# Kernel tuning notes

Measured on AMD Instinct MI355X. Metric: run time of the kernel, lower is better.

## Reference

```python
import jax, jax.numpy as jnp
import numpy as np

N = 40962  # icosphere level-6 vertex count
EPS = 1e-5

def setup_inputs() -> dict:
    key = jax.random.key(0)
    ks = jax.random.split(key, 8)
    x = jax.random.normal(ks[0], (N, 3), dtype=jnp.float32)
    neigh_orders = jax.random.randint(ks[1], (N * 7,), 0, N, dtype=jnp.int32)
    s0 = 1.0 / np.sqrt(21.0)
    sm = 1.0 / np.sqrt(896.0)
    return {
        "x": x,
        "neigh_orders": neigh_orders,
        "W0": jax.random.uniform(ks[2], (21, 128), jnp.float32, -s0, s0),
        "b0": jax.random.uniform(ks[3], (128,), jnp.float32, -s0, s0),
        "g0": jnp.ones((128,), jnp.float32),
        "be0": jnp.zeros((128,), jnp.float32),
        "Wm": jax.random.uniform(ks[4], (14, 896, 128), jnp.float32, -sm, sm),
        "bm": jax.random.uniform(ks[5], (14, 128), jnp.float32, -sm, sm),
        "gm": jnp.ones((14, 128), jnp.float32),
        "bem": jnp.zeros((14, 128), jnp.float32),
        "Wl": jax.random.uniform(ks[6], (896, 36), jnp.float32, -sm, sm),
        "bl": jax.random.uniform(ks[7], (36,), jnp.float32, -sm, sm),
    }

def _bs(x, idx, W, b):
    # gather 7 fixed ring neighbors per node, flatten, dense linear
    mat = x[idx].reshape(x.shape[0], -1)  # [N, 7*in_feats]
    return mat @ W + b

def _bn_train(h, g, be):
    # BatchNorm1d in training mode: biased variance over the node/batch dim
    mu = jnp.mean(h, axis=0)
    var = jnp.var(h, axis=0)
    return g * (h - mu) * jax.lax.rsqrt(var + EPS) + be

def reference(x, neigh_orders, W0, b0, g0, be0, Wm, bm, gm, bem, Wl, bl):
    idx = neigh_orders
    h = jax.nn.relu(_bn_train(_bs(x, idx, W0, b0), g0, be0))  # [N, 128]

    def step(h, params):
        W, b, g, be = params
        h = jax.nn.relu(_bn_train(_bs(h, idx, W, b), g, be))
        return h, None

    h, _ = jax.lax.scan(step, h, (Wm, bm, gm, bem))  # 14 identical 128->128 blocks
    out = _bs(h, idx, Wl, bl)  # [N, num_classes]
    return out
```

## Files before the change

### kernel.cpp

```cpp
#include <hip/hip_runtime.h>

typedef _Float16 f16x8 __attribute__((ext_vector_type(8)));
typedef float f32x4 __attribute__((ext_vector_type(4)));

#define EPS 1e-5f

__device__ __forceinline__ short f2h(float x) {
    _Float16 h = (_Float16)x;
    union { _Float16 h; short s; } u;
    u.h = h;
    return u.s;
}

__global__ void prep_kernel(const float* __restrict__ Wm, const float* __restrict__ Wl,
                            short* __restrict__ WtM, short* __restrict__ WtF,
                            float* __restrict__ stats) {
    const long T1 = 14L * 896 * 128;
    const long T2 = 48L * 896;
    const long T3 = 15L * 256;
    long i = (long)blockIdx.x * blockDim.x + threadIdx.x;
    if (i < T1) {
        long l = i / (896 * 128);
        long r = i % (896 * 128);
        long k = r >> 7;
        long f = r & 127;
        WtM[l * 114688 + f * 896 + k] = f2h(Wm[i]);
    } else if (i < T1 + T2) {
        long j = i - T1;
        long f = j / 896;
        long k = j % 896;
        WtF[j] = (f < 36) ? f2h(Wl[k * 36 + f]) : (short)0;
    } else if (i < T1 + T2 + T3) {
        stats[i - T1 - T2] = 0.0f;
    }
}

#define L0_NB 16
__global__ __launch_bounds__(256) void layer0_kernel(
        const float* __restrict__ x, const int* __restrict__ idx,
        const float* __restrict__ W0, const float* __restrict__ b0,
        short* __restrict__ hlin, float* __restrict__ stats, int N) {
    __shared__ float sW[21 * 128];
    __shared__ float sX[L0_NB * 21];
    __shared__ float sStat[256];
    const int tid = threadIdx.x;
    for (int i = tid; i < 21 * 128; i += 256) sW[i] = W0[i];
    const int f = tid & 127;
    const int half = tid >> 7;
    const float bf = b0[f];
    float s = 0.f, ss = 0.f;
    const int ntiles = (N + L0_NB - 1) / L0_NB;
    for (int t = blockIdx.x; t < ntiles; t += gridDim.x) {
        const int n0 = t * L0_NB;
        __syncthreads();
        for (int i = tid; i < L0_NB * 21; i += 256) {
            int ni = i / 21;
            int k = i - ni * 21;
            int j = k / 3;
            int c = k - j * 3;
            int n = n0 + ni;
            if (n >= N) n = N - 1;
            sX[i] = x[(long)idx[n * 7 + j] * 3 + c];
        }
        __syncthreads();
#pragma unroll
        for (int ni = 0; ni < 8; ++ni) {
            int node = n0 + half * 8 + ni;
            if (node >= N) break;
            float acc = bf;
#pragma unroll
            for (int k = 0; k < 21; ++k)
                acc = fmaf(sX[(half * 8 + ni) * 21 + k], sW[k * 128 + f], acc);
            hlin[(long)node * 128 + f] = f2h(acc);
            s += acc;
            ss += acc * acc;
        }
    }
    __syncthreads();
    if (half == 1) { sStat[f] = s; sStat[128 + f] = ss; }
    __syncthreads();
    if (half == 0) {
        atomicAdd(&stats[f], s + sStat[f]);
        atomicAdd(&stats[128 + f], ss + sStat[128 + f]);
    }
}

__global__ __launch_bounds__(256, 3) void gemm_mid_kernel(
        const short* __restrict__ hprev, const int* __restrict__ idx,
        const short* __restrict__ Wt, const float* __restrict__ bvec,
        const float* __restrict__ g, const float* __restrict__ be,
        const float* __restrict__ statsIn,
        short* __restrict__ hlin, float* __restrict__ statsOut,
        int N, float invN) {
    __shared__ short sA[64 * 136];
    __shared__ short sB[128 * 136];
    __shared__ float sAux[256];

    const int tid = threadIdx.x;
    const int wave = tid >> 6;
    const int lane = tid & 63;
    const int quad = lane >> 4;
    const int l16 = lane & 15;
    const int wm = wave & 1;
    const int wf = wave >> 1;
    const int m0 = blockIdx.x * 64;
    const int t16 = tid >> 4;
    const int fb = (tid & 15) * 8;

    if (tid < 128) {
        float mu = statsIn[tid] * invN;
        float var = statsIn[128 + tid] * invN - mu * mu;
        float rs = rsqrtf(var + EPS);
        float sc = g[tid] * rs;
        sAux[tid] = sc;
        sAux[128 + tid] = be[tid] - mu * sc;
    }
    __syncthreads();
    float scR[8], shR[8];
#pragma unroll
    for (int e = 0; e < 8; ++e) {
        scR[e] = sAux[fb + e];
        shR[e] = sAux[128 + fb + e];
    }

    f32x4 acc[2][4];
#pragma unroll
    for (int ni = 0; ni < 4; ++ni) {
        float bv0 = bvec[wf * 64 + ni * 16 + l16];
#pragma unroll
        for (int mi = 0; mi < 2; ++mi) {
            acc[mi][ni][0] = bv0; acc[mi][ni][1] = bv0; acc[mi][ni][2] = bv0; acc[mi][ni][3] = bv0;
        }
    }

    f16x8 av[4];
    f16x8 bv[8];

    auto issueA = [&](int j) {
#pragma unroll
        for (int it = 0; it < 4; ++it) {
            int nl = t16 + it * 16;
            int n = m0 + nl;
            n = (n < N) ? n : (N - 1);
            long row = idx[n * 7 + j];
            av[it] = *(const f16x8*)&hprev[row * 128 + fb];
        }
    };
    auto issueB = [&](int j) {
#pragma unroll
        for (int it = 0; it < 8; ++it) {
            int ff = t16 + it * 16;
            bv[it] = *(const f16x8*)&Wt[(long)ff * 896 + j * 128 + fb];
        }
    };
    auto writeA = [&]() {
#pragma unroll
        for (int it = 0; it < 4; ++it) {
            int nl = t16 + it * 16;
            f16x8 hv = av[it];
            union { short sh8[8]; f16x8 v; } u;
#pragma unroll
            for (int e = 0; e < 8; ++e) {
                float v = (float)hv[e];
                u.sh8[e] = f2h(fmaxf(fmaf(v, scR[e], shR[e]), 0.f));
            }
            *(f16x8*)&sA[nl * 136 + fb] = u.v;
        }
    };
    auto writeB = [&]() {
#pragma unroll
        for (int it = 0; it < 8; ++it) {
            int ff = t16 + it * 16;
            *(f16x8*)&sB[ff * 136 + fb] = bv[it];
        }
    };

    issueB(0);
    issueA(0);

    for (int j = 0; j < 7; ++j) {
        __syncthreads();
        writeB();
        writeA();
        if (j < 6) {
            issueB(j + 1);
            issueA(j + 1);
        }
        __syncthreads();
#pragma unroll
        for (int k0 = 0; k0 < 128; k0 += 32) {
            f16x8 a[2], b[4];
#pragma unroll
            for (int mi = 0; mi < 2; ++mi)
                a[mi] = *(const f16x8*)&sA[(wm * 32 + mi * 16 + l16) * 136 + k0 + quad * 8];
#pragma unroll
            for (int ni = 0; ni < 4; ++ni)
                b[ni] = *(const f16x8*)&sB[(wf * 64 + ni * 16 + l16) * 136 + k0 + quad * 8];
#pragma unroll
            for (int mi = 0; mi < 2; ++mi)
#pragma unroll
                for (int ni = 0; ni < 4; ++ni)
                    acc[mi][ni] = __builtin_amdgcn_mfma_f32_16x16x32_f16(a[mi], b[ni], acc[mi][ni], 0, 0, 0);
        }
    }

    __syncthreads();
    sAux[tid] = 0.f;
    __syncthreads();
#pragma unroll
    for (int mi = 0; mi < 2; ++mi) {
#pragma unroll
        for (int ni = 0; ni < 4; ++ni) {
            int feat = wf * 64 + ni * 16 + l16;
            float s = 0.f, ss = 0.f;
#pragma unroll
            for (int r = 0; r < 4; ++r) {
                int node = m0 + wm * 32 + mi * 16 + quad * 4 + r;
                float v = acc[mi][ni][r];
                if (node < N) {
                    hlin[(long)node * 128 + feat] = f2h(v);
                    s += v;
                    ss += v * v;
                }
            }
            atomicAdd(&sAux[feat], s);
            atomicAdd(&sAux[128 + feat], ss);
        }
    }
    __syncthreads();
    if (tid < 128) {
        atomicAdd(&statsOut[tid], sAux[tid]);
        atomicAdd(&statsOut[128 + tid], sAux[128 + tid]);
    }
}

__global__ __launch_bounds__(256) void gemm_final_kernel(
        const short* __restrict__ hprev, const int* __restrict__ idx,
        const short* __restrict__ WtF, const float* __restrict__ bl,
        const float* __restrict__ g, const float* __restrict__ be,
        const float* __restrict__ statsIn,
        float* __restrict__ out, int N, float invN) {
    __shared__ short sA[64 * 136];
    __shared__ short sB[48 * 136];
    __shared__ float sAux[256];

    const int tid = threadIdx.x;
    const int wave = tid >> 6;
    const int lane = tid & 63;
    const int quad = lane >> 4;
    const int l16 = lane & 15;
    const int m0 = blockIdx.x * 64;
    const int t16 = tid >> 4;
    const int fb = (tid & 15) * 8;

    if (tid < 128) {
        float mu = statsIn[tid] * invN;
        float var = statsIn[128 + tid] * invN - mu * mu;
        float rs = rsqrtf(var + EPS);
        float sc = g[tid] * rs;
        sAux[tid] = sc;
        sAux[128 + tid] = be[tid] - mu * sc;
    }
    __syncthreads();
    float scR[8], shR[8];
#pragma unroll
    for (int e = 0; e < 8; ++e) {
        scR[e] = sAux[fb + e];
        shR[e] = sAux[128 + fb + e];
    }

    f32x4 acc[3];
#pragma unroll
    for (int ni = 0; ni < 3; ++ni) {
        int feat = ni * 16 + l16;
        float bv0 = (feat < 36) ? bl[feat] : 0.f;
        acc[ni][0] = bv0; acc[ni][1] = bv0; acc[ni][2] = bv0; acc[ni][3] = bv0;
    }

    f16x8 av[4];
    f16x8 bv[3];

    auto issueA = [&](int j) {
#pragma unroll
        for (int it = 0; it < 4; ++it) {
            int nl = t16 + it * 16;
            int n = m0 + nl;
            n = (n < N) ? n : (N - 1);
            long row = idx[n * 7 + j];
            av[it] = *(const f16x8*)&hprev[row * 128 + fb];
        }
    };
    auto issueB = [&](int j) {
#pragma unroll
        for (int it = 0; it < 3; ++it) {
            int ff = t16 + it * 16;
            bv[it] = *(const f16x8*)&WtF[(long)ff * 896 + j * 128 + fb];
        }
    };
    auto writeA = [&]() {
#pragma unroll
        for (int it = 0; it < 4; ++it) {
            int nl = t16 + it * 16;
            f16x8 hv = av[it];
            union { short sh8[8]; f16x8 v; } u;
#pragma unroll
            for (int e = 0; e < 8; ++e) {
                float v = (float)hv[e];
                u.sh8[e] = f2h(fmaxf(fmaf(v, scR[e], shR[e]), 0.f));
            }
            *(f16x8*)&sA[nl * 136 + fb] = u.v;
        }
    };
    auto writeB = [&]() {
#pragma unroll
        for (int it = 0; it < 3; ++it) {
            int ff = t16 + it * 16;
            *(f16x8*)&sB[ff * 136 + fb] = bv[it];
        }
    };

    issueB(0);
    issueA(0);

    for (int j = 0; j < 7; ++j) {
        __syncthreads();
        writeB();
        writeA();
        if (j < 6) {
            issueB(j + 1);
            issueA(j + 1);
        }
        __syncthreads();
#pragma unroll
        for (int k0 = 0; k0 < 128; k0 += 32) {
            f16x8 a = *(const f16x8*)&sA[(wave * 16 + l16) * 136 + k0 + quad * 8];
            f16x8 b[3];
#pragma unroll
            for (int ni = 0; ni < 3; ++ni)
                b[ni] = *(const f16x8*)&sB[(ni * 16 + l16) * 136 + k0 + quad * 8];
#pragma unroll
            for (int ni = 0; ni < 3; ++ni)
                acc[ni] = __builtin_amdgcn_mfma_f32_16x16x32_f16(a, b[ni], acc[ni], 0, 0, 0);
        }
    }

#pragma unroll
    for (int ni = 0; ni < 3; ++ni) {
        int feat = ni * 16 + l16;
        if (feat < 36) {
#pragma unroll
            for (int r = 0; r < 4; ++r) {
                int node = m0 + wave * 16 + quad * 4 + r;
                if (node < N) out[(long)node * 36 + feat] = acc[ni][r];
            }
        }
    }
}

extern "C" void kernel_launch(void* const* d_in, const int* in_sizes, int n_in,
                              void* d_out, int out_size, void* d_ws, size_t ws_size,
                              hipStream_t stream) {
    const float* x   = (const float*)d_in[0];
    const int*   idx = (const int*)d_in[1];
    const float* W0  = (const float*)d_in[2];
    const float* b0  = (const float*)d_in[3];
    const float* g0  = (const float*)d_in[4];
    const float* be0 = (const float*)d_in[5];
    const float* Wm  = (const float*)d_in[6];
    const float* bm  = (const float*)d_in[7];
    const float* gm  = (const float*)d_in[8];
    const float* bem = (const float*)d_in[9];
    const float* Wl  = (const float*)d_in[10];
    const float* bl  = (const float*)d_in[11];
    float* out = (float*)d_out;

    const int N = in_sizes[0] / 3;
    const float invN = 1.0f / (float)N;

    char* ws = (char*)d_ws;
    size_t off = 0;
    auto alloc = [&](size_t bytes) -> void* {
        void* p = ws + off;
        off = (off + bytes + 255) & ~(size_t)255;
        return p;
    };
    short* WtM   = (short*)alloc(14UL * 128 * 896 * 2);
    short* WtF   = (short*)alloc(48UL * 896 * 2);
    float* stats = (float*)alloc(15UL * 256 * 4);
    short* hlinA = (short*)alloc((size_t)N * 128 * 2);
    short* hlinB = (short*)alloc((size_t)N * 128 * 2);

    {
        long total = 14L * 896 * 128 + 48L * 896 + 15L * 256;
        int blocks = (int)((total + 255) / 256);
        prep_kernel<<<blocks, 256, 0, stream>>>(Wm, Wl, WtM, WtF, stats);
    }

    layer0_kernel<<<1280, 256, 0, stream>>>(x, idx, W0, b0, hlinA, stats, N);

    const int gblocks = (N + 63) / 64;
    short* hin = hlinA;
    short* hout = hlinB;
    const float* gPrev = g0;
    const float* bePrev = be0;
    for (int L = 0; L < 14; ++L) {
        gemm_mid_kernel<<<gblocks, 256, 0, stream>>>(
            hin, idx, WtM + (size_t)L * 128 * 896, bm + L * 128,
            gPrev, bePrev, stats + L * 256,
            hout, stats + (L + 1) * 256, N, invN);
        gPrev = gm + L * 128;
        bePrev = bem + L * 128;
        short* t = hin; hin = hout; hout = t;
    }

    gemm_final_kernel<<<gblocks, 256, 0, stream>>>(
        hin, idx, WtF, bl, gm + 13 * 128, bem + 13 * 128, stats + 14 * 256,
        out, N, invN);
}
```

Measured before the change: 733.7 us.

## Split mid GEMM output features across two blocks and keep layer0 weights in registers

Each mid-layer GEMM block now computes only 64 of the 128 output features for its 64-node tile, which doubles the grid and halves the B tile, accumulators and shared memory. The launch bound is raised to 4 blocks per SM to improve occupancy and latency hiding. The cost is that each gathered A tile (with its BN+ReLU applied) is now fetched and transformed twice. Layer0 keeps its weight column in registers instead of shared memory and launches one block per tile instead of a grid-strided loop.

```diff
diff --git a/kernel.cpp b/kernel.cpp
--- a/kernel.cpp
+++ b/kernel.cpp
@@ -40,13 +40,14 @@
         const float* __restrict__ x, const int* __restrict__ idx,
         const float* __restrict__ W0, const float* __restrict__ b0,
         short* __restrict__ hlin, float* __restrict__ stats, int N) {
-    __shared__ float sW[21 * 128];
     __shared__ float sX[L0_NB * 21];
     __shared__ float sStat[256];
     const int tid = threadIdx.x;
-    for (int i = tid; i < 21 * 128; i += 256) sW[i] = W0[i];
     const int f = tid & 127;
     const int half = tid >> 7;
+    float wreg[21];
+#pragma unroll
+    for (int k = 0; k < 21; ++k) wreg[k] = W0[k * 128 + f];
     const float bf = b0[f];
     float s = 0.f, ss = 0.f;
     const int ntiles = (N + L0_NB - 1) / L0_NB;
@@ -70,7 +71,7 @@
             float acc = bf;
 #pragma unroll
             for (int k = 0; k < 21; ++k)
-                acc = fmaf(sX[(half * 8 + ni) * 21 + k], sW[k * 128 + f], acc);
+                acc = fmaf(sX[(half * 8 + ni) * 21 + k], wreg[k], acc);
             hlin[(long)node * 128 + f] = f2h(acc);
             s += acc;
             ss += acc * acc;
@@ -85,7 +86,7 @@
     }
 }
 
-__global__ __launch_bounds__(256, 3) void gemm_mid_kernel(
+__global__ __launch_bounds__(256, 4) void gemm_mid_kernel(
         const short* __restrict__ hprev, const int* __restrict__ idx,
         const short* __restrict__ Wt, const float* __restrict__ bvec,
         const float* __restrict__ g, const float* __restrict__ be,
@@ -93,7 +94,7 @@
         short* __restrict__ hlin, float* __restrict__ statsOut,
         int N, float invN) {
     __shared__ short sA[64 * 136];
-    __shared__ short sB[128 * 136];
+    __shared__ short sB[64 * 136];
     __shared__ float sAux[256];
 
     const int tid = threadIdx.x;
@@ -103,7 +104,10 @@
     const int l16 = lane & 15;
     const int wm = wave & 1;
     const int wf = wave >> 1;
-    const int m0 = blockIdx.x * 64;
+    const int tile = blockIdx.x >> 1;
+    const int fg = blockIdx.x & 1;
+    const int m0 = tile * 64;
+    const int f0 = fg * 64;
     const int t16 = tid >> 4;
     const int fb = (tid & 15) * 8;
 
@@ -123,10 +127,10 @@
         shR[e] = sAux[128 + fb + e];
     }
 
-    f32x4 acc[2][4];
-#pragma unroll
-    for (int ni = 0; ni < 4; ++ni) {
-        float bv0 = bvec[wf * 64 + ni * 16 + l16];
+    f32x4 acc[2][2];
+#pragma unroll
+    for (int ni = 0; ni < 2; ++ni) {
+        float bv0 = bvec[f0 + wf * 32 + ni * 16 + l16];
 #pragma unroll
         for (int mi = 0; mi < 2; ++mi) {
             acc[mi][ni][0] = bv0; acc[mi][ni][1] = bv0; acc[mi][ni][2] = bv0; acc[mi][ni][3] = bv0;
@@ -134,7 +138,7 @@
     }
 
     f16x8 av[4];
-    f16x8 bv[8];
+    f16x8 bv[4];
 
     auto issueA = [&](int j) {
 #pragma unroll
@@ -148,8 +152,8 @@
     };
     auto issueB = [&](int j) {
 #pragma unroll
-        for (int it = 0; it < 8; ++it) {
-            int ff = t16 + it * 16;
+        for (int it = 0; it < 4; ++it) {
+            int ff = f0 + t16 + it * 16;
             bv[it] = *(const f16x8*)&Wt[(long)ff * 896 + j * 128 + fb];
         }
     };
@@ -169,9 +173,9 @@
     };
     auto writeB = [&]() {
 #pragma unroll
-        for (int it = 0; it < 8; ++it) {
-            int ff = t16 + it * 16;
-            *(f16x8*)&sB[ff * 136 + fb] = bv[it];
+        for (int it = 0; it < 4; ++it) {
+            int ffl = t16 + it * 16;
+            *(f16x8*)&sB[ffl * 136 + fb] = bv[it];
         }
     };
 
@@ -189,48 +193,48 @@
         __syncthreads();
 #pragma unroll
         for (int k0 = 0; k0 < 128; k0 += 32) {
-            f16x8 a[2], b[4];
+            f16x8 a[2], b[2];
 #pragma unroll
             for (int mi = 0; mi < 2; ++mi)
                 a[mi] = *(const f16x8*)&sA[(wm * 32 + mi * 16 + l16) * 136 + k0 + quad * 8];
 #pragma unroll
-            for (int ni = 0; ni < 4; ++ni)
-                b[ni] = *(const f16x8*)&sB[(wf * 64 + ni * 16 + l16) * 136 + k0 + quad * 8];
+            for (int ni = 0; ni < 2; ++ni)
+                b[ni] = *(const f16x8*)&sB[(wf * 32 + ni * 16 + l16) * 136 + k0 + quad * 8];
 #pragma unroll
             for (int mi = 0; mi < 2; ++mi)
 #pragma unroll
-                for (int ni = 0; ni < 4; ++ni)
+                for (int ni = 0; ni < 2; ++ni)
                     acc[mi][ni] = __builtin_amdgcn_mfma_f32_16x16x32_f16(a[mi], b[ni], acc[mi][ni], 0, 0, 0);
         }
     }
 
     __syncthreads();
-    sAux[tid] = 0.f;
-    __syncthreads();
-#pragma unroll
-    for (int mi = 0; mi < 2; ++mi) {
-#pragma unroll
-        for (int ni = 0; ni < 4; ++ni) {
-            int feat = wf * 64 + ni * 16 + l16;
-            float s = 0.f, ss = 0.f;
+    if (tid < 128) sAux[tid] = 0.f;
+    __syncthreads();
+#pragma unroll
+    for (int ni = 0; ni < 2; ++ni) {
+        int lf = wf * 32 + ni * 16 + l16;
+        float s = 0.f, ss = 0.f;
+#pragma unroll
+        for (int mi = 0; mi < 2; ++mi) {
 #pragma unroll
             for (int r = 0; r < 4; ++r) {
                 int node = m0 + wm * 32 + mi * 16 + quad * 4 + r;
                 float v = acc[mi][ni][r];
                 if (node < N) {
-                    hlin[(long)node * 128 + feat] = f2h(v);
+                    hlin[(long)node * 128 + f0 + lf] = f2h(v);
                     s += v;
                     ss += v * v;
                 }
             }
-            atomicAdd(&sAux[feat], s);
-            atomicAdd(&sAux[128 + feat], ss);
-        }
-    }
-    __syncthreads();
-    if (tid < 128) {
-        atomicAdd(&statsOut[tid], sAux[tid]);
-        atomicAdd(&statsOut[128 + tid], sAux[128 + tid]);
+        }
+        atomicAdd(&sAux[lf], s);
+        atomicAdd(&sAux[64 + lf], ss);
+    }
+    __syncthreads();
+    if (tid < 64) {
+        atomicAdd(&statsOut[f0 + tid], sAux[tid]);
+        atomicAdd(&statsOut[128 + f0 + tid], sAux[64 + tid]);
     }
 }
 
@@ -396,15 +400,16 @@
         prep_kernel<<<blocks, 256, 0, stream>>>(Wm, Wl, WtM, WtF, stats);
     }
 
-    layer0_kernel<<<1280, 256, 0, stream>>>(x, idx, W0, b0, hlinA, stats, N);
-
-    const int gblocks = (N + 63) / 64;
+    const int ntiles0 = (N + L0_NB - 1) / L0_NB;
+    layer0_kernel<<<ntiles0, 256, 0, stream>>>(x, idx, W0, b0, hlinA, stats, N);
+
+    const int gblocks_mid = ((N + 63) / 64) * 2;
     short* hin = hlinA;
     short* hout = hlinB;
     const float* gPrev = g0;
     const float* bePrev = be0;
     for (int L = 0; L < 14; ++L) {
-        gemm_mid_kernel<<<gblocks, 256, 0, stream>>>(
+        gemm_mid_kernel<<<gblocks_mid, 256, 0, stream>>>(
             hin, idx, WtM + (size_t)L * 128 * 896, bm + L * 128,
             gPrev, bePrev, stats + L * 256,
             hout, stats + (L + 1) * 256, N, invN);
@@ -413,7 +418,8 @@
         short* t = hin; hin = hout; hout = t;
     }
 
-    gemm_final_kernel<<<gblocks, 256, 0, stream>>>(
+    const int gblocks_fin = (N + 63) / 64;
+    gemm_final_kernel<<<gblocks_fin, 256, 0, stream>>>(
         hin, idx, WtF, bl, gm + 13 * 128, bem + 13 * 128, stats + 14 * 256,
         out, N, invN);
 }
```

After: 641.3 us. 1.14x faster.
